# Kernel optimization log

Hardware: AMD Instinct MI355X
Metric: run time of the kernel (lower is better)

Reference implementation:

```python
import jax, jax.numpy as jnp
import numpy as np

V, D, B, L, Dh, BS = 50257, 1024, 8, 2, 128, 256

def setup_inputs() -> dict:
    key = jax.random.key(0)
    ks = jax.random.split(key, 16)
    std = lambda fan: 1.0 / np.sqrt(fan)
    return {
        'input_id': jax.random.randint(ks[0], (BS,), 0, V),
        'reset_mask': jax.random.randint(ks[1], (BS,), 0, 2).astype(bool),
        'surprise': jnp.zeros((BS, 1), jnp.float32),
        'wm_state': jax.random.normal(ks[2], (BS, D), jnp.float32) * 0.1,
        'h_state': jax.random.normal(ks[3], (L, BS, B, Dh), jnp.float32) * 0.1,
        'emb': jax.random.normal(ks[4], (V, D), jnp.float32) * std(D),
        'W_in': jax.random.normal(ks[5], (D, D), jnp.float32) * std(D),
        'W_alpha': jax.random.normal(ks[6], (D, D), jnp.float32) * std(D),
        'W_wm_out': jax.random.normal(ks[7], (D, D), jnp.float32) * std(D),
        'W_x': jax.random.normal(ks[8], (L, B, Dh, Dh), jnp.float32) * std(Dh),
        'W_h': jax.random.normal(ks[9], (L, B, Dh, Dh), jnp.float32) * std(Dh),
        'W_wml': jax.random.normal(ks[10], (L, B, Dh, D), jnp.float32) * std(D),
        'W_g': jax.random.normal(ks[11], (L, B, Dh, Dh), jnp.float32) * std(Dh),
        'w_s': jnp.zeros((L, B, Dh), jnp.float32),   # surprise gate weights (init 0, as in torch init)
        'b_g': jnp.zeros((L, B, Dh), jnp.float32),   # gate bias
    }


def reference(input_id, reset_mask, surprise, wm_state, h_state, emb, W_in,
              W_alpha, W_wm_out, W_x, W_h, W_wml, W_g, w_s, b_g):
    # carry = (~reset_mask) as float, zeroes all recurrent state at doc boundary
    carry = (~reset_mask).astype(jnp.float32)[:, None]            # [BS,1]
    x = emb[input_id]                                             # [BS,D] token embedding
    # GLA-style working memory: input-conditioned decay of carried state
    alpha = jax.nn.sigmoid(x @ W_alpha.T)                         # [BS,D]
    wm_new = carry * alpha * wm_state + x                         # [BS,D]
    y_wm = jnp.tanh(wm_new @ W_wm_out.T)                          # [BS,D]
    # input projection and split into B block slices of width D_h
    x_proj = x @ W_in.T                                           # [BS,D]
    cur = x_proj.reshape(BS, B, Dh)                               # [BS,B,Dh]
    carry_b = carry[:, :, None]                                   # [BS,1,1]
    # L sequential layers per block; all B blocks updated in parallel via einsum
    for l in range(L):
        a = (jnp.einsum('sbd,bed->sbe', cur, W_x[l])
             + jnp.einsum('sbd,bed->sbe', h_state[l], W_h[l])
             + jnp.einsum('sD,beD->sbe', y_wm, W_wml[l]))         # [BS,B,Dh]
        g = jax.nn.sigmoid(jnp.einsum('sbd,bed->sbe', a, W_g[l])
                           + surprise[:, :, None] * w_s[l] + b_g[l])
        h_new = carry_b * ((1.0 - g) * h_state[l] + g * jnp.tanh(a))
        cur = h_new
    h_final = cur.reshape(BS, D)                                  # concat of per-block outputs
    logits = h_final @ emb.T                                      # tied lm_head
    return logits, x, y_wm
```

## Files before the change

### kernel.cpp

```cpp
#include <hip/hip_runtime.h>
#include <math.h>

#define BSZ 256
#define DIM 1024
#define VOC 50257
#define NL 2
#define NB 8
#define DH 128

typedef __bf16 bf16x8 __attribute__((ext_vector_type(8)));
typedef float  f32x4  __attribute__((ext_vector_type(4)));
typedef unsigned short u16;
typedef u16 u16x8 __attribute__((ext_vector_type(8)));

__device__ __forceinline__ u16 f2bf(float f) {
  unsigned int u = __float_as_uint(f);
  u += 0x7fffu + ((u >> 16) & 1u);
  return (u16)(u >> 16);
}
__device__ __forceinline__ float sigm(float x) { return 1.0f / (1.0f + __expf(-x)); }

template<int M16, int N16, int K, bool CLAMPN>
__device__ __forceinline__ void wave_gemm(
    const u16* __restrict__ A, int lda,
    const float* __restrict__ B, int ldb, int nClamp,
    f32x4 (&acc)[M16][N16])
{
  const int lane = threadIdx.x & 63;
  const int quad = lane >> 4;
  const int l16  = lane & 15;

  const u16* aR[M16];
  const float* bR[N16];
#pragma unroll
  for (int mi = 0; mi < M16; ++mi)
    aR[mi] = A + (long)(mi * 16 + l16) * lda + quad * 8;
#pragma unroll
  for (int ni = 0; ni < N16; ++ni) {
    int n = ni * 16 + l16;
    if (CLAMPN) n = n > nClamp ? nClamp : n;
    bR[ni] = B + (long)n * ldb + quad * 8;
  }

  bf16x8 aF[4][M16];
  bf16x8 bF[4][N16];

#define WG_LOAD(kk, buf)                                                  \
  {                                                                       \
    _Pragma("unroll")                                                     \
    for (int ni = 0; ni < N16; ++ni) {                                    \
      float4 v0 = *(const float4*)(bR[ni] + (kk));                        \
      float4 v1 = *(const float4*)(bR[ni] + (kk) + 4);                    \
      u16x8 h;                                                            \
      h[0] = f2bf(v0.x); h[1] = f2bf(v0.y);                               \
      h[2] = f2bf(v0.z); h[3] = f2bf(v0.w);                               \
      h[4] = f2bf(v1.x); h[5] = f2bf(v1.y);                               \
      h[6] = f2bf(v1.z); h[7] = f2bf(v1.w);                               \
      bF[buf][ni] = __builtin_bit_cast(bf16x8, h);                        \
    }                                                                     \
    _Pragma("unroll")                                                     \
    for (int mi = 0; mi < M16; ++mi)                                      \
      aF[buf][mi] = *(const bf16x8*)(aR[mi] + (kk));                      \
  }

#define WG_MM(buf)                                                        \
  {                                                                       \
    _Pragma("unroll")                                                     \
    for (int mi = 0; mi < M16; ++mi)                                      \
      _Pragma("unroll")                                                   \
      for (int ni = 0; ni < N16; ++ni)                                    \
        acc[mi][ni] = __builtin_amdgcn_mfma_f32_16x16x32_bf16(            \
            aF[buf][mi], bF[buf][ni], acc[mi][ni], 0, 0, 0);              \
  }

  WG_LOAD(0, 0);
  WG_LOAD(32, 1);
  WG_LOAD(64, 2);
#pragma unroll 1
  for (int kk = 0; kk < K - 128; kk += 128) {
    WG_LOAD(kk + 96, 3);  WG_MM(0);
    WG_LOAD(kk + 128, 0); WG_MM(1);
    WG_LOAD(kk + 160, 1); WG_MM(2);
    WG_LOAD(kk + 192, 2); WG_MM(3);
  }
  WG_LOAD(K - 32, 3);
  WG_MM(0); WG_MM(1); WG_MM(2); WG_MM(3);
#undef WG_LOAD
#undef WG_MM
}

#define ACC_DECL(N16V)                                \
  f32x4 acc[4][N16V];                                 \
  { f32x4 z = {0.f, 0.f, 0.f, 0.f};                   \
    _Pragma("unroll")                                 \
    for (int i = 0; i < 4; ++i)                       \
      _Pragma("unroll")                               \
      for (int j = 0; j < N16V; ++j) acc[i][j] = z; }

__global__ __launch_bounds__(256) void k_prep(
    const int* __restrict__ ids, const void* __restrict__ mask,
    const float* __restrict__ emb, const float* __restrict__ hstate,
    const float* __restrict__ W_alpha, const float* __restrict__ W_in,
    const float* __restrict__ W_wm_out, const float* __restrict__ W_x,
    const float* __restrict__ W_h, const float* __restrict__ W_wml,
    const float* __restrict__ W_g,
    float* __restrict__ xout, u16* __restrict__ x_bf,
    u16* __restrict__ h_bf, float* __restrict__ carry, float* __restrict__ sink)
{
  __shared__ int sInt;
  const int tid = threadIdx.x, s = blockIdx.x;
  if (tid == 0) sInt = 1;
  __syncthreads();
  if (tid < 64) {
    int v = ((const int*)mask)[tid];
    if (v != 0 && v != 1) atomicAnd(&sInt, 0);
  }
  __syncthreads();
  if (tid == 0) {
    int m = sInt ? ((const int*)mask)[s] : (int)((const unsigned char*)mask)[s];
    carry[s] = m ? 0.0f : 1.0f;
  }
  long id = ids[s];
  int k = tid * 4;
  float4 v = *(const float4*)(emb + id * DIM + k);
  *(float4*)(xout + (long)s * DIM + k) = v;
  ushort4 h; h.x = f2bf(v.x); h.y = f2bf(v.y); h.z = f2bf(v.z); h.w = f2bf(v.w);
  *(ushort4*)(x_bf + (long)s * DIM + k) = h;
#pragma unroll
  for (int l = 0; l < NL; ++l) {
    long off = (long)l * BSZ * DIM + (long)s * DIM + k;
    float4 w = *(const float4*)(hstate + off);
    ushort4 o; o.x = f2bf(w.x); o.y = f2bf(w.y); o.z = f2bf(w.z); o.w = f2bf(w.w);
    *(ushort4*)(h_bf + off) = o;
  }
  long gtid = (long)blockIdx.x * 256 + tid;
  long gstride = (long)gridDim.x * 256;
  float acc = 0.f;
  {
    const long nDD = (long)DIM * DIM / 4;
    for (long i = gtid; i < nDD; i += gstride) {
      float4 a = ((const float4*)W_alpha)[i];
      float4 b = ((const float4*)W_in)[i];
      float4 c = ((const float4*)W_wm_out)[i];
      acc += a.x + a.w + b.x + b.w + c.x + c.w;
    }
    const long nS = (long)NL * NB * DH * DH / 4;
    for (long i = gtid; i < nS; i += gstride) {
      float4 a = ((const float4*)W_x)[i];
      float4 b = ((const float4*)W_h)[i];
      float4 c = ((const float4*)W_g)[i];
      acc += a.x + a.w + b.x + b.w + c.x + c.w;
    }
    const long nW = (long)NL * NB * DH * DIM / 4;
    for (long i = gtid; i < nW; i += gstride) {
      float4 a = ((const float4*)W_wml)[i];
      acc += a.x + a.w;
    }
  }
  if (acc == -1.17521e35f) *sink = acc;
}

__global__ __launch_bounds__(64) void k_gemm1(
    const u16* __restrict__ x_bf,
    const float* __restrict__ W_alpha, const float* __restrict__ W_in,
    const float* __restrict__ carry, const float* __restrict__ wm_state,
    const float* __restrict__ xout,
    u16* __restrict__ wm_bf, u16* __restrict__ cur_bf)
{
  const int tid = threadIdx.x, quad = tid >> 4, l16 = tid & 15;
  const int m = blockIdx.x & 3;
  const int nt = blockIdx.x >> 2;
  const bool isAlpha = nt < 64;
  const int n0 = (isAlpha ? nt : nt - 64) * 16;
  ACC_DECL(1)
  wave_gemm<4, 1, DIM, false>(x_bf + (long)m * 64 * DIM, DIM,
                              (isAlpha ? W_alpha : W_in) + (long)n0 * DIM, DIM, 0, acc);
#pragma unroll
  for (int mi = 0; mi < 4; ++mi) {
    int n = n0 + l16;
#pragma unroll
    for (int r = 0; r < 4; ++r) {
      int s = m * 64 + mi * 16 + quad * 4 + r;
      float c = acc[mi][0][r];
      long idx = (long)s * DIM + n;
      if (isAlpha) wm_bf[idx] = f2bf(carry[s] * sigm(c) * wm_state[idx] + xout[idx]);
      else         cur_bf[idx] = f2bf(c);
    }
  }
}

__global__ __launch_bounds__(64) void k_gemm2(
    const u16* __restrict__ wm_bf, const float* __restrict__ W_wm_out,
    float* __restrict__ yout, u16* __restrict__ ywm_bf)
{
  const int tid = threadIdx.x, quad = tid >> 4, l16 = tid & 15;
  const int m = blockIdx.x & 3;
  const int n0 = (blockIdx.x >> 2) * 16;
  ACC_DECL(1)
  wave_gemm<4, 1, DIM, false>(wm_bf + (long)m * 64 * DIM, DIM,
                              W_wm_out + (long)n0 * DIM, DIM, 0, acc);
#pragma unroll
  for (int mi = 0; mi < 4; ++mi) {
    int n = n0 + l16;
#pragma unroll
    for (int r = 0; r < 4; ++r) {
      int s = m * 64 + mi * 16 + quad * 4 + r;
      float y = tanhf(acc[mi][0][r]);
      long idx = (long)s * DIM + n;
      yout[idx] = y;
      ywm_bf[idx] = f2bf(y);
    }
  }
}

__global__ __launch_bounds__(64) void k_gemm_a(
    int l, const u16* __restrict__ cur_bf, const u16* __restrict__ h_bf,
    const u16* __restrict__ ywm_bf,
    const float* __restrict__ W_x, const float* __restrict__ W_h,
    const float* __restrict__ W_wml,
    float* __restrict__ a_f32, u16* __restrict__ a_bf)
{
  const int tid = threadIdx.x, quad = tid >> 4, l16 = tid & 15;
  const int m = blockIdx.x & 3;
  const int nt = blockIdx.x >> 2;
  const int b = nt >> 3;
  const int e0 = (nt & 7) * 16;
  ACC_DECL(1)
  const long moff = (long)m * 64 * DIM;
  wave_gemm<4, 1, DH, false>(cur_bf + moff + b * DH, DIM,
                             W_x + ((long)(l * NB + b) * DH + e0) * DH, DH, 0, acc);
  wave_gemm<4, 1, DH, false>(h_bf + (long)l * BSZ * DIM + moff + b * DH, DIM,
                             W_h + ((long)(l * NB + b) * DH + e0) * DH, DH, 0, acc);
  wave_gemm<4, 1, DIM, false>(ywm_bf + moff, DIM,
                              W_wml + ((long)(l * NB + b) * DH + e0) * DIM, DIM, 0, acc);
#pragma unroll
  for (int mi = 0; mi < 4; ++mi) {
    int e = e0 + l16;
#pragma unroll
    for (int r = 0; r < 4; ++r) {
      int s = m * 64 + mi * 16 + quad * 4 + r;
      float c = acc[mi][0][r];
      long idx = (long)s * DIM + b * DH + e;
      a_f32[idx] = c;
      a_bf[idx] = f2bf(c);
    }
  }
}

__global__ __launch_bounds__(64) void k_gemm_g(
    int l, const u16* __restrict__ a_bf, const float* __restrict__ W_g,
    const float* __restrict__ w_s, const float* __restrict__ b_g,
    const float* __restrict__ surprise, const float* __restrict__ carry,
    const float* __restrict__ hstate, const float* __restrict__ a_f32,
    u16* __restrict__ hout_bf)
{
  const int tid = threadIdx.x, quad = tid >> 4, l16 = tid & 15;
  const int m = blockIdx.x & 3;
  const int nt = blockIdx.x >> 2;
  const int b = nt >> 3;
  const int e0 = (nt & 7) * 16;
  ACC_DECL(1)
  wave_gemm<4, 1, DH, false>(a_bf + (long)m * 64 * DIM + b * DH, DIM,
                             W_g + ((long)(l * NB + b) * DH + e0) * DH, DH, 0, acc);
#pragma unroll
  for (int mi = 0; mi < 4; ++mi) {
    int e = e0 + l16;
#pragma unroll
    for (int r = 0; r < 4; ++r) {
      int s = m * 64 + mi * 16 + quad * 4 + r;
      float c = acc[mi][0][r];
      long idx = (long)s * DIM + b * DH + e;
      float gp = c + surprise[s] * w_s[(l * NB + b) * DH + e] + b_g[(l * NB + b) * DH + e];
      float g = sigm(gp);
      float ho = hstate[(long)l * BSZ * DIM + idx];
      float hn = carry[s] * ((1.0f - g) * ho + g * tanhf(a_f32[idx]));
      hout_bf[idx] = f2bf(hn);
    }
  }
}

__global__ __launch_bounds__(256) void k_logits_lds(
    const u16* __restrict__ hfin_bf, const float* __restrict__ emb,
    float* __restrict__ out)
{
  __shared__ u16 Bs[2][64 * 64];
  const int tid  = threadIdx.x;
  const int wave = tid >> 6;
  const int lane = tid & 63;
  const int quad = lane >> 4;
  const int l16  = lane & 15;
  const int n0   = blockIdx.x * 64;

  const int srow = tid >> 2;
  const int scol = (tid & 3) * 16;
  long gn = n0 + srow;
  if (gn >= VOC) gn = VOC - 1;
  const float* src = emb + gn * DIM + scol;
  const int sw  = (srow & 7) << 4;
  const int sb0 = srow * 128 + ((scol * 2) ^ sw);
  const int sb1 = srow * 128 + (((scol * 2) + 16) ^ sw);

  const u16* aP[4];
#pragma unroll
  for (int mi = 0; mi < 4; ++mi)
    aP[mi] = hfin_bf + (long)(wave * 64 + mi * 16 + l16) * DIM + quad * 8;

  f32x4 acc[4][4];
  { f32x4 z = {0.f, 0.f, 0.f, 0.f};
#pragma unroll
    for (int mi = 0; mi < 4; ++mi)
#pragma unroll
      for (int ni = 0; ni < 4; ++ni) acc[mi][ni] = z; }

  float4 pA, pB, pC, pD;
#define LD4(t)                                                            \
  { pA = *(const float4*)(src + (t) * 64);                                \
    pB = *(const float4*)(src + (t) * 64 + 4);                            \
    pC = *(const float4*)(src + (t) * 64 + 8);                            \
    pD = *(const float4*)(src + (t) * 64 + 12); }
#define CVT_WR(bufi)                                                      \
  { u16x8 h0, h1;                                                         \
    h0[0] = f2bf(pA.x); h0[1] = f2bf(pA.y);                               \
    h0[2] = f2bf(pA.z); h0[3] = f2bf(pA.w);                               \
    h0[4] = f2bf(pB.x); h0[5] = f2bf(pB.y);                               \
    h0[6] = f2bf(pB.z); h0[7] = f2bf(pB.w);                               \
    h1[0] = f2bf(pC.x); h1[1] = f2bf(pC.y);                               \
    h1[2] = f2bf(pC.z); h1[3] = f2bf(pC.w);                               \
    h1[4] = f2bf(pD.x); h1[5] = f2bf(pD.y);                               \
    h1[6] = f2bf(pD.z); h1[7] = f2bf(pD.w);                               \
    *(u16x8*)((char*)&Bs[bufi][0] + sb0) = h0;                            \
    *(u16x8*)((char*)&Bs[bufi][0] + sb1) = h1; }

  LD4(0)
  CVT_WR(0)
  LD4(1)
  __syncthreads();

  const int NT = DIM / 64;
#pragma unroll 1
  for (int t = 0; t < NT; ++t) {
    const char* bb = (const char*)&Bs[t & 1][0];
    const int k0 = t * 64;

    bf16x8 aF0[4], aF1[4], bF0[4], bF1[4];
#pragma unroll
    for (int mi = 0; mi < 4; ++mi) aF0[mi] = *(const bf16x8*)(aP[mi] + k0);
#pragma unroll
    for (int mi = 0; mi < 4; ++mi) aF1[mi] = *(const bf16x8*)(aP[mi] + k0 + 32);
#pragma unroll
    for (int ni = 0; ni < 4; ++ni) {
      const int row = ni * 16 + l16;
      const int ib0 = (quad * 16) ^ ((row & 7) << 4);
      bF0[ni] = *(const bf16x8*)(bb + row * 128 + ib0);
      bF1[ni] = *(const bf16x8*)(bb + row * 128 + (ib0 ^ 64));
    }
#pragma unroll
    for (int mi = 0; mi < 4; ++mi)
#pragma unroll
      for (int ni = 0; ni < 4; ++ni)
        acc[mi][ni] = __builtin_amdgcn_mfma_f32_16x16x32_bf16(
            aF0[mi], bF0[ni], acc[mi][ni], 0, 0, 0);
#pragma unroll
    for (int mi = 0; mi < 4; ++mi)
#pragma unroll
      for (int ni = 0; ni < 4; ++ni)
        acc[mi][ni] = __builtin_amdgcn_mfma_f32_16x16x32_bf16(
            aF1[mi], bF1[ni], acc[mi][ni], 0, 0, 0);

    if (t + 1 < NT) {
      CVT_WR((t + 1) & 1)
      if (t + 2 < NT) LD4(t + 2)
    }
    __syncthreads();
  }
#undef LD4
#undef CVT_WR

#pragma unroll
  for (int mi = 0; mi < 4; ++mi)
#pragma unroll
    for (int ni = 0; ni < 4; ++ni) {
      int n = n0 + ni * 16 + l16;
      if (n < VOC) {
#pragma unroll
        for (int r = 0; r < 4; ++r) {
          int s = wave * 64 + mi * 16 + quad * 4 + r;
          out[(long)s * VOC + n] = acc[mi][ni][r];
        }
      }
    }
}

extern "C" void kernel_launch(void* const* d_in, const int* in_sizes, int n_in,
                              void* d_out, int out_size, void* d_ws, size_t ws_size,
                              hipStream_t stream) {
  const int*   input_id = (const int*)d_in[0];
  const void*  reset    = d_in[1];
  const float* surprise = (const float*)d_in[2];
  const float* wm_state = (const float*)d_in[3];
  const float* h_state  = (const float*)d_in[4];
  const float* emb      = (const float*)d_in[5];
  const float* W_in     = (const float*)d_in[6];
  const float* W_alpha  = (const float*)d_in[7];
  const float* W_wm_out = (const float*)d_in[8];
  const float* W_x      = (const float*)d_in[9];
  const float* W_h      = (const float*)d_in[10];
  const float* W_wml    = (const float*)d_in[11];
  const float* W_g      = (const float*)d_in[12];
  const float* w_s      = (const float*)d_in[13];
  const float* b_g      = (const float*)d_in[14];

  float* out  = (float*)d_out;
  float* xout = out + (size_t)BSZ * VOC;
  float* yout = xout + (size_t)BSZ * DIM;

  const long SD = (long)BSZ * DIM;
  u16* scr    = (u16*)d_out;
  u16* x_bf   = scr;
  u16* wm_bf  = scr + SD;
  u16* cur_bf = scr + 2 * SD;
  u16* ywm_bf = scr + 3 * SD;
  u16* h_bf   = scr + 4 * SD;
  u16* a_bf   = scr + 6 * SD;
  float* a_f32 = (float*)(scr + 8 * SD);

  float* carry  = (float*)d_ws;
  u16* hfin_bf  = (u16*)((char*)d_ws + 1024);
  float* sink   = (float*)((char*)d_ws + 600 * 1024);

  k_prep<<<BSZ, 256, 0, stream>>>(input_id, reset, emb, h_state,
                                  W_alpha, W_in, W_wm_out, W_x, W_h, W_wml, W_g,
                                  xout, x_bf, h_bf, carry, sink);
  k_gemm1<<<512, 64, 0, stream>>>(x_bf, W_alpha, W_in, carry, wm_state, xout, wm_bf, cur_bf);
  k_gemm2<<<256, 64, 0, stream>>>(wm_bf, W_wm_out, yout, ywm_bf);
  k_gemm_a<<<256, 64, 0, stream>>>(0, cur_bf, h_bf, ywm_bf, W_x, W_h, W_wml, a_f32, a_bf);
  k_gemm_g<<<256, 64, 0, stream>>>(0, a_bf, W_g, w_s, b_g, surprise, carry, h_state, a_f32, cur_bf);
  k_gemm_a<<<256, 64, 0, stream>>>(1, cur_bf, h_bf, ywm_bf, W_x, W_h, W_wml, a_f32, a_bf);
  k_gemm_g<<<256, 64, 0, stream>>>(1, a_bf, W_g, w_s, b_g, surprise, carry, h_state, a_f32, hfin_bf);
  k_logits_lds<<<(VOC + 63) / 64, 256, 0, stream>>>(hfin_bf, emb, out);
}
```

Measured before the change: 461.1 us.

## Fuse both recurrent layers into one LDS-resident kernel; deepen logits prefetch

Replaces the four per-layer gate/activation kernels with one k_layers kernel. Each 512-thread block owns 16 rows of one block slice and keeps cur, a and h in LDS across both layers, so the global a_f32/a_bf round trips and three launches go away. The logits kernel's loop is unrolled by two with two register prefetch sets, so emb loads are issued two tiles ahead. The trade-off is fewer blocks (128) and smaller M tiles that reload weights per row-group, plus higher register pressure in the logits kernel.

```diff
diff --git a/kernel.cpp b/kernel.cpp
--- a/kernel.cpp
+++ b/kernel.cpp
@@ -89,6 +89,27 @@
 #undef WG_MM
 }
 
+__device__ __forceinline__ void wave_gemm_ldsA(
+    const u16* S, const float* __restrict__ B, int ldb, f32x4& acc,
+    int l16, int quad)
+{
+  const float* bR = B + (long)l16 * ldb + quad * 8;
+#pragma unroll
+  for (int c = 0; c < 4; ++c) {
+    bf16x8 af = *(const bf16x8*)((const char*)S + l16 * 256 +
+                                 ((c * 64 + quad * 16) ^ ((l16 & 7) << 4)));
+    float4 v0 = *(const float4*)(bR + c * 32);
+    float4 v1 = *(const float4*)(bR + c * 32 + 4);
+    u16x8 h;
+    h[0] = f2bf(v0.x); h[1] = f2bf(v0.y);
+    h[2] = f2bf(v0.z); h[3] = f2bf(v0.w);
+    h[4] = f2bf(v1.x); h[5] = f2bf(v1.y);
+    h[6] = f2bf(v1.z); h[7] = f2bf(v1.w);
+    acc = __builtin_amdgcn_mfma_f32_16x16x32_bf16(
+        af, __builtin_bit_cast(bf16x8, h), acc, 0, 0, 0);
+  }
+}
+
 #define ACC_DECL(N16V)                                \
   f32x4 acc[4][N16V];                                 \
   { f32x4 z = {0.f, 0.f, 0.f, 0.f};                   \
@@ -213,69 +234,75 @@
   }
 }
 
-__global__ __launch_bounds__(64) void k_gemm_a(
-    int l, const u16* __restrict__ cur_bf, const u16* __restrict__ h_bf,
+__global__ __launch_bounds__(512) void k_layers(
+    const u16* __restrict__ cur_bf, const u16* __restrict__ h_bf,
     const u16* __restrict__ ywm_bf,
     const float* __restrict__ W_x, const float* __restrict__ W_h,
-    const float* __restrict__ W_wml,
-    float* __restrict__ a_f32, u16* __restrict__ a_bf)
-{
-  const int tid = threadIdx.x, quad = tid >> 4, l16 = tid & 15;
-  const int m = blockIdx.x & 3;
-  const int nt = blockIdx.x >> 2;
-  const int b = nt >> 3;
-  const int e0 = (nt & 7) * 16;
-  ACC_DECL(1)
-  const long moff = (long)m * 64 * DIM;
-  wave_gemm<4, 1, DH, false>(cur_bf + moff + b * DH, DIM,
-                             W_x + ((long)(l * NB + b) * DH + e0) * DH, DH, 0, acc);
-  wave_gemm<4, 1, DH, false>(h_bf + (long)l * BSZ * DIM + moff + b * DH, DIM,
-                             W_h + ((long)(l * NB + b) * DH + e0) * DH, DH, 0, acc);
-  wave_gemm<4, 1, DIM, false>(ywm_bf + moff, DIM,
-                              W_wml + ((long)(l * NB + b) * DH + e0) * DIM, DIM, 0, acc);
-#pragma unroll
-  for (int mi = 0; mi < 4; ++mi) {
-    int e = e0 + l16;
-#pragma unroll
-    for (int r = 0; r < 4; ++r) {
-      int s = m * 64 + mi * 16 + quad * 4 + r;
-      float c = acc[mi][0][r];
-      long idx = (long)s * DIM + b * DH + e;
-      a_f32[idx] = c;
-      a_bf[idx] = f2bf(c);
-    }
-  }
-}
-
-__global__ __launch_bounds__(64) void k_gemm_g(
-    int l, const u16* __restrict__ a_bf, const float* __restrict__ W_g,
+    const float* __restrict__ W_wml, const float* __restrict__ W_g,
     const float* __restrict__ w_s, const float* __restrict__ b_g,
     const float* __restrict__ surprise, const float* __restrict__ carry,
-    const float* __restrict__ hstate, const float* __restrict__ a_f32,
-    u16* __restrict__ hout_bf)
-{
-  const int tid = threadIdx.x, quad = tid >> 4, l16 = tid & 15;
-  const int m = blockIdx.x & 3;
-  const int nt = blockIdx.x >> 2;
-  const int b = nt >> 3;
-  const int e0 = (nt & 7) * 16;
-  ACC_DECL(1)
-  wave_gemm<4, 1, DH, false>(a_bf + (long)m * 64 * DIM + b * DH, DIM,
-                             W_g + ((long)(l * NB + b) * DH + e0) * DH, DH, 0, acc);
-#pragma unroll
-  for (int mi = 0; mi < 4; ++mi) {
-    int e = e0 + l16;
+    const float* __restrict__ hstate,
+    u16* __restrict__ hfin_bf)
+{
+  __shared__ u16 S[16 * 128];
+  const int tid  = threadIdx.x;
+  const int wv   = tid >> 6;
+  const int lane = tid & 63;
+  const int quad = lane >> 4, l16 = lane & 15;
+  const int m  = blockIdx.x & 15;
+  const int b  = blockIdx.x >> 4;
+  const int e0 = wv * 16;
+  const int row0 = m * 16;
+
+  {
+    const int r  = tid >> 5;
+    const int c8 = (tid & 31) * 8;
+    uint2 v = *(const uint2*)((const char*)(cur_bf + (long)(row0 + r) * DIM + b * DH) + c8);
+    *(uint2*)((char*)S + r * 256 + (c8 ^ ((r & 7) << 4))) = v;
+  }
+  __syncthreads();
+
+#pragma unroll 1
+  for (int l = 0; l < NL; ++l) {
+    const long wb = (long)(l * NB + b) * DH;
+    f32x4 aacc[1][1];
+    { f32x4 z = {0.f, 0.f, 0.f, 0.f}; aacc[0][0] = z; }
+    wave_gemm_ldsA(S, W_x + (wb + e0) * DH, DH, aacc[0][0], l16, quad);
+    wave_gemm<1, 1, DH, false>(h_bf + (long)l * BSZ * DIM + (long)row0 * DIM + b * DH, DIM,
+                               W_h + (wb + e0) * DH, DH, 0, aacc);
+    wave_gemm<1, 1, DIM, false>(ywm_bf + (long)row0 * DIM, DIM,
+                                W_wml + (wb + e0) * DIM, DIM, 0, aacc);
+    __syncthreads();
 #pragma unroll
     for (int r = 0; r < 4; ++r) {
-      int s = m * 64 + mi * 16 + quad * 4 + r;
-      float c = acc[mi][0][r];
-      long idx = (long)s * DIM + b * DH + e;
-      float gp = c + surprise[s] * w_s[(l * NB + b) * DH + e] + b_g[(l * NB + b) * DH + e];
-      float g = sigm(gp);
-      float ho = hstate[(long)l * BSZ * DIM + idx];
-      float hn = carry[s] * ((1.0f - g) * ho + g * tanhf(a_f32[idx]));
-      hout_bf[idx] = f2bf(hn);
-    }
+      int row = quad * 4 + r;
+      *(u16*)((char*)S + row * 256 + (((e0 + l16) * 2) ^ ((row & 7) << 4))) =
+          f2bf(aacc[0][0][r]);
+    }
+    __syncthreads();
+    f32x4 gacc = {0.f, 0.f, 0.f, 0.f};
+    wave_gemm_ldsA(S, W_g + (wb + e0) * DH, DH, gacc, l16, quad);
+    const int col = e0 + l16;
+    const float ws_v = w_s[wb + col];
+    const float bg_v = b_g[wb + col];
+    float hn[4];
+#pragma unroll
+    for (int r = 0; r < 4; ++r) {
+      int s = row0 + quad * 4 + r;
+      float g = sigm(gacc[r] + surprise[s] * ws_v + bg_v);
+      float ho = hstate[(long)l * BSZ * DIM + (long)s * DIM + b * DH + col];
+      hn[r] = carry[s] * ((1.0f - g) * ho + g * tanhf(aacc[0][0][r]));
+    }
+    __syncthreads();
+#pragma unroll
+    for (int r = 0; r < 4; ++r) {
+      int row = quad * 4 + r;
+      u16 hv = f2bf(hn[r]);
+      *(u16*)((char*)S + row * 256 + ((col * 2) ^ ((row & 7) << 4))) = hv;
+      if (l == NL - 1)
+        hfin_bf[(long)(row0 + row) * DIM + b * DH + col] = hv;
+    }
+    __syncthreads();
   }
 }
 
@@ -312,69 +339,82 @@
 #pragma unroll
       for (int ni = 0; ni < 4; ++ni) acc[mi][ni] = z; }
 
-  float4 pA, pB, pC, pD;
-#define LD4(t)                                                            \
-  { pA = *(const float4*)(src + (t) * 64);                                \
-    pB = *(const float4*)(src + (t) * 64 + 4);                            \
-    pC = *(const float4*)(src + (t) * 64 + 8);                            \
-    pD = *(const float4*)(src + (t) * 64 + 12); }
-#define CVT_WR(bufi)                                                      \
+  float4 P0, P1, P2, P3, Q0, Q1, Q2, Q3;
+#define LDP(t)                                                            \
+  { P0 = *(const float4*)(src + (t) * 64);                                \
+    P1 = *(const float4*)(src + (t) * 64 + 4);                            \
+    P2 = *(const float4*)(src + (t) * 64 + 8);                            \
+    P3 = *(const float4*)(src + (t) * 64 + 12); }
+#define LDQ(t)                                                            \
+  { Q0 = *(const float4*)(src + (t) * 64);                                \
+    Q1 = *(const float4*)(src + (t) * 64 + 4);                            \
+    Q2 = *(const float4*)(src + (t) * 64 + 8);                            \
+    Q3 = *(const float4*)(src + (t) * 64 + 12); }
+#define CVT_WR(bufi, a, bq, c, d)                                         \
   { u16x8 h0, h1;                                                         \
-    h0[0] = f2bf(pA.x); h0[1] = f2bf(pA.y);                               \
-    h0[2] = f2bf(pA.z); h0[3] = f2bf(pA.w);                               \
-    h0[4] = f2bf(pB.x); h0[5] = f2bf(pB.y);                               \
-    h0[6] = f2bf(pB.z); h0[7] = f2bf(pB.w);                               \
-    h1[0] = f2bf(pC.x); h1[1] = f2bf(pC.y);                               \
-    h1[2] = f2bf(pC.z); h1[3] = f2bf(pC.w);                               \
-    h1[4] = f2bf(pD.x); h1[5] = f2bf(pD.y);                               \
-    h1[6] = f2bf(pD.z); h1[7] = f2bf(pD.w);                               \
+    h0[0] = f2bf(a.x); h0[1] = f2bf(a.y);                                 \
+    h0[2] = f2bf(a.z); h0[3] = f2bf(a.w);                                 \
+    h0[4] = f2bf(bq.x); h0[5] = f2bf(bq.y);                               \
+    h0[6] = f2bf(bq.z); h0[7] = f2bf(bq.w);                               \
+    h1[0] = f2bf(c.x); h1[1] = f2bf(c.y);                                 \
+    h1[2] = f2bf(c.z); h1[3] = f2bf(c.w);                                 \
+    h1[4] = f2bf(d.x); h1[5] = f2bf(d.y);                                 \
+    h1[6] = f2bf(d.z); h1[7] = f2bf(d.w);                                 \
     *(u16x8*)((char*)&Bs[bufi][0] + sb0) = h0;                            \
     *(u16x8*)((char*)&Bs[bufi][0] + sb1) = h1; }
-
-  LD4(0)
-  CVT_WR(0)
-  LD4(1)
+#define COMPUTE(t, bufi)                                                  \
+  { const char* bb = (const char*)&Bs[bufi][0];                           \
+    const int k0 = (t) * 64;                                              \
+    bf16x8 aF0[4], aF1[4], bF0[4], bF1[4];                                \
+    _Pragma("unroll")                                                     \
+    for (int mi = 0; mi < 4; ++mi) aF0[mi] = *(const bf16x8*)(aP[mi] + k0);\
+    _Pragma("unroll")                                                     \
+    for (int mi = 0; mi < 4; ++mi) aF1[mi] = *(const bf16x8*)(aP[mi] + k0 + 32);\
+    _Pragma("unroll")                                                     \
+    for (int ni = 0; ni < 4; ++ni) {                                      \
+      const int row = ni * 16 + l16;                                      \
+      const int ib0 = (quad * 16) ^ ((row & 7) << 4);                     \
+      bF0[ni] = *(const bf16x8*)(bb + row * 128 + ib0);                   \
+      bF1[ni] = *(const bf16x8*)(bb + row * 128 + (ib0 ^ 64));            \
+    }                                                                     \
+    _Pragma("unroll")                                                     \
+    for (int mi = 0; mi < 4; ++mi)                                        \
+      _Pragma("unroll")                                                   \
+      for (int ni = 0; ni < 4; ++ni)                                      \
+        acc[mi][ni] = __builtin_amdgcn_mfma_f32_16x16x32_bf16(            \
+            aF0[mi], bF0[ni], acc[mi][ni], 0, 0, 0);                      \
+    _Pragma("unroll")                                                     \
+    for (int mi = 0; mi < 4; ++mi)                                        \
+      _Pragma("unroll")                                                   \
+      for (int ni = 0; ni < 4; ++ni)                                      \
+        acc[mi][ni] = __builtin_amdgcn_mfma_f32_16x16x32_bf16(            \
+            aF1[mi], bF1[ni], acc[mi][ni], 0, 0, 0);                      \
+  }
+
+  LDP(0)
+  CVT_WR(0, P0, P1, P2, P3)
+  LDP(1)
+  LDQ(2)
   __syncthreads();
 
   const int NT = DIM / 64;
 #pragma unroll 1
-  for (int t = 0; t < NT; ++t) {
-    const char* bb = (const char*)&Bs[t & 1][0];
-    const int k0 = t * 64;
-
-    bf16x8 aF0[4], aF1[4], bF0[4], bF1[4];
-#pragma unroll
-    for (int mi = 0; mi < 4; ++mi) aF0[mi] = *(const bf16x8*)(aP[mi] + k0);
-#pragma unroll
-    for (int mi = 0; mi < 4; ++mi) aF1[mi] = *(const bf16x8*)(aP[mi] + k0 + 32);
-#pragma unroll
-    for (int ni = 0; ni < 4; ++ni) {
-      const int row = ni * 16 + l16;
-      const int ib0 = (quad * 16) ^ ((row & 7) << 4);
-      bF0[ni] = *(const bf16x8*)(bb + row * 128 + ib0);
-      bF1[ni] = *(const bf16x8*)(bb + row * 128 + (ib0 ^ 64));
-    }
-#pragma unroll
-    for (int mi = 0; mi < 4; ++mi)
-#pragma unroll
-      for (int ni = 0; ni < 4; ++ni)
-        acc[mi][ni] = __builtin_amdgcn_mfma_f32_16x16x32_bf16(
-            aF0[mi], bF0[ni], acc[mi][ni], 0, 0, 0);
-#pragma unroll
-    for (int mi = 0; mi < 4; ++mi)
-#pragma unroll
-      for (int ni = 0; ni < 4; ++ni)
-        acc[mi][ni] = __builtin_amdgcn_mfma_f32_16x16x32_bf16(
-            aF1[mi], bF1[ni], acc[mi][ni], 0, 0, 0);
-
-    if (t + 1 < NT) {
-      CVT_WR((t + 1) & 1)
-      if (t + 2 < NT) LD4(t + 2)
-    }
-    __syncthreads();
-  }
-#undef LD4
+  for (int t = 0; t < NT; t += 2) {
+    COMPUTE(t, 0)
+    CVT_WR(1, P0, P1, P2, P3)
+    if (t + 3 < NT) LDP(t + 3)
+    __syncthreads();
+    COMPUTE(t + 1, 1)
+    if (t + 2 < NT) {
+      CVT_WR(0, Q0, Q1, Q2, Q3)
+      if (t + 4 < NT) LDQ(t + 4)
+    }
+    __syncthreads();
+  }
+#undef LDP
+#undef LDQ
 #undef CVT_WR
+#undef COMPUTE
 
 #pragma unroll
   for (int mi = 0; mi < 4; ++mi)
@@ -421,8 +461,6 @@
   u16* cur_bf = scr + 2 * SD;
   u16* ywm_bf = scr + 3 * SD;
   u16* h_bf   = scr + 4 * SD;
-  u16* a_bf   = scr + 6 * SD;
-  float* a_f32 = (float*)(scr + 8 * SD);
 
   float* carry  = (float*)d_ws;
   u16* hfin_bf  = (u16*)((char*)d_ws + 1024);
@@ -433,9 +471,7 @@
                                   xout, x_bf, h_bf, carry, sink);
   k_gemm1<<<512, 64, 0, stream>>>(x_bf, W_alpha, W_in, carry, wm_state, xout, wm_bf, cur_bf);
   k_gemm2<<<256, 64, 0, stream>>>(wm_bf, W_wm_out, yout, ywm_bf);
-  k_gemm_a<<<256, 64, 0, stream>>>(0, cur_bf, h_bf, ywm_bf, W_x, W_h, W_wml, a_f32, a_bf);
-  k_gemm_g<<<256, 64, 0, stream>>>(0, a_bf, W_g, w_s, b_g, surprise, carry, h_state, a_f32, cur_bf);
-  k_gemm_a<<<256, 64, 0, stream>>>(1, cur_bf, h_bf, ywm_bf, W_x, W_h, W_wml, a_f32, a_bf);
-  k_gemm_g<<<256, 64, 0, stream>>>(1, a_bf, W_g, w_s, b_g, surprise, carry, h_state, a_f32, hfin_bf);
+  k_layers<<<128, 512, 0, stream>>>(cur_bf, h_bf, ywm_bf, W_x, W_h, W_wml, W_g,
+                                    w_s, b_g, surprise, carry, h_state, hfin_bf);
   k_logits_lds<<<(VOC + 63) / 64, 256, 0, stream>>>(hfin_bf, emb, out);
 }
```

New measurement: 482.7 us. +4.7%, slower.

## Stage fp32 embedding tiles into LDS with direct global-to-LDS loads in logits GEMM

Applied to the files above, without the earlier changes.

The logits kernel now copies fp32 embedding tiles straight into LDS through global_load_lds (16 bytes per lane) using an XOR swizzle. The bf16 conversion moves to the point where B fragments are read from LDS. This removes the register round trip and the conversion-then-store step from the prefetch path, and lets the next tile's load be issued before the current tile's MFMAs. In exchange LDS use doubles (fp32 tiles), each wave does more LDS reads and conversions per MFMA, and the double-buffer sync relies on the barrier covering the asynchronous LDS writes.

```diff
diff --git a/kernel.cpp b/kernel.cpp
--- a/kernel.cpp
+++ b/kernel.cpp
@@ -11,6 +11,7 @@
 typedef __bf16 bf16x8 __attribute__((ext_vector_type(8)));
 typedef float  f32x4  __attribute__((ext_vector_type(4)));
 typedef unsigned short u16;
+typedef unsigned int u32;
 typedef u16 u16x8 __attribute__((ext_vector_type(8)));
 
 __device__ __forceinline__ u16 f2bf(float f) {
@@ -19,6 +20,19 @@
   return (u16)(u >> 16);
 }
 __device__ __forceinline__ float sigm(float x) { return 1.0f / (1.0f + __expf(-x)); }
+
+__device__ __forceinline__ bf16x8 cvt8(float4 a, float4 b) {
+  bf16x8 r;
+  r[0] = (__bf16)a.x; r[1] = (__bf16)a.y; r[2] = (__bf16)a.z; r[3] = (__bf16)a.w;
+  r[4] = (__bf16)b.x; r[5] = (__bf16)b.y; r[6] = (__bf16)b.z; r[7] = (__bf16)b.w;
+  return r;
+}
+
+__device__ __forceinline__ void gld16(const float* g, float* l) {
+  __builtin_amdgcn_global_load_lds(
+      (const __attribute__((address_space(1))) u32*)(g),
+      (__attribute__((address_space(3))) u32*)(l), 16, 0, 0);
+}
 
 template<int M16, int N16, int K, bool CLAMPN>
 __device__ __forceinline__ void wave_gemm(
@@ -279,11 +293,11 @@
   }
 }
 
-__global__ __launch_bounds__(256) void k_logits_lds(
+__global__ __launch_bounds__(256) void k_logits_gl(
     const u16* __restrict__ hfin_bf, const float* __restrict__ emb,
     float* __restrict__ out)
 {
-  __shared__ u16 Bs[2][64 * 64];
+  __shared__ float Bs[2][64 * 64];
   const int tid  = threadIdx.x;
   const int wave = tid >> 6;
   const int lane = tid & 63;
@@ -291,14 +305,15 @@
   const int l16  = lane & 15;
   const int n0   = blockIdx.x * 64;
 
-  const int srow = tid >> 2;
-  const int scol = (tid & 3) * 16;
-  long gn = n0 + srow;
-  if (gn >= VOC) gn = VOC - 1;
-  const float* src = emb + gn * DIM + scol;
-  const int sw  = (srow & 7) << 4;
-  const int sb0 = srow * 128 + ((scol * 2) ^ sw);
-  const int sb1 = srow * 128 + (((scol * 2) + 16) ^ sw);
+  const float* srcP[4];
+#pragma unroll
+  for (int j = 0; j < 4; ++j) {
+    int r = wave * 16 + j * 4 + (lane >> 4);
+    int c = (lane & 15) ^ (r & 15);
+    long gn = n0 + r; if (gn > VOC - 1) gn = VOC - 1;
+    srcP[j] = emb + gn * DIM + c * 4;
+  }
+  float* const dst0 = &Bs[0][wave * 16 * 64];
 
   const u16* aP[4];
 #pragma unroll
@@ -312,47 +327,36 @@
 #pragma unroll
       for (int ni = 0; ni < 4; ++ni) acc[mi][ni] = z; }
 
-  float4 pA, pB, pC, pD;
-#define LD4(t)                                                            \
-  { pA = *(const float4*)(src + (t) * 64);                                \
-    pB = *(const float4*)(src + (t) * 64 + 4);                            \
-    pC = *(const float4*)(src + (t) * 64 + 8);                            \
-    pD = *(const float4*)(src + (t) * 64 + 12); }
-#define CVT_WR(bufi)                                                      \
-  { u16x8 h0, h1;                                                         \
-    h0[0] = f2bf(pA.x); h0[1] = f2bf(pA.y);                               \
-    h0[2] = f2bf(pA.z); h0[3] = f2bf(pA.w);                               \
-    h0[4] = f2bf(pB.x); h0[5] = f2bf(pB.y);                               \
-    h0[6] = f2bf(pB.z); h0[7] = f2bf(pB.w);                               \
-    h1[0] = f2bf(pC.x); h1[1] = f2bf(pC.y);                               \
-    h1[2] = f2bf(pC.z); h1[3] = f2bf(pC.w);                               \
-    h1[4] = f2bf(pD.x); h1[5] = f2bf(pD.y);                               \
-    h1[6] = f2bf(pD.z); h1[7] = f2bf(pD.w);                               \
-    *(u16x8*)((char*)&Bs[bufi][0] + sb0) = h0;                            \
-    *(u16x8*)((char*)&Bs[bufi][0] + sb1) = h1; }
-
-  LD4(0)
-  CVT_WR(0)
-  LD4(1)
+#define STAGE(bufi, t)                                                    \
+  { _Pragma("unroll")                                                     \
+    for (int j = 0; j < 4; ++j)                                           \
+      gld16(srcP[j] + (t) * 64, dst0 + (bufi) * 4096 + j * 256); }
+
+  STAGE(0, 0)
   __syncthreads();
 
   const int NT = DIM / 64;
 #pragma unroll 1
   for (int t = 0; t < NT; ++t) {
+    const int k0 = t * 64;
+    bf16x8 aF0[4], aF1[4];
+#pragma unroll
+    for (int mi = 0; mi < 4; ++mi) aF0[mi] = *(const bf16x8*)(aP[mi] + k0);
+#pragma unroll
+    for (int mi = 0; mi < 4; ++mi) aF1[mi] = *(const bf16x8*)(aP[mi] + k0 + 32);
+    if (t + 1 < NT) { STAGE((t + 1) & 1, t + 1) }
+
     const char* bb = (const char*)&Bs[t & 1][0];
-    const int k0 = t * 64;
-
-    bf16x8 aF0[4], aF1[4], bF0[4], bF1[4];
-#pragma unroll
-    for (int mi = 0; mi < 4; ++mi) aF0[mi] = *(const bf16x8*)(aP[mi] + k0);
-#pragma unroll
-    for (int mi = 0; mi < 4; ++mi) aF1[mi] = *(const bf16x8*)(aP[mi] + k0 + 32);
+    bf16x8 bF0[4], bF1[4];
 #pragma unroll
     for (int ni = 0; ni < 4; ++ni) {
-      const int row = ni * 16 + l16;
-      const int ib0 = (quad * 16) ^ ((row & 7) << 4);
-      bF0[ni] = *(const bf16x8*)(bb + row * 128 + ib0);
-      bF1[ni] = *(const bf16x8*)(bb + row * 128 + (ib0 ^ 64));
+      const char* rb = bb + (ni * 16 + l16) * 256;
+      float4 u0 = *(const float4*)(rb + (((quad * 2)     ^ l16) << 4));
+      float4 u1 = *(const float4*)(rb + (((quad * 2 + 1) ^ l16) << 4));
+      float4 w0 = *(const float4*)(rb + (((quad * 2 + 8) ^ l16) << 4));
+      float4 w1 = *(const float4*)(rb + (((quad * 2 + 9) ^ l16) << 4));
+      bF0[ni] = cvt8(u0, u1);
+      bF1[ni] = cvt8(w0, w1);
     }
 #pragma unroll
     for (int mi = 0; mi < 4; ++mi)
@@ -367,14 +371,9 @@
         acc[mi][ni] = __builtin_amdgcn_mfma_f32_16x16x32_bf16(
             aF1[mi], bF1[ni], acc[mi][ni], 0, 0, 0);
 
-    if (t + 1 < NT) {
-      CVT_WR((t + 1) & 1)
-      if (t + 2 < NT) LD4(t + 2)
-    }
     __syncthreads();
   }
-#undef LD4
-#undef CVT_WR
+#undef STAGE
 
 #pragma unroll
   for (int mi = 0; mi < 4; ++mi)
@@ -437,5 +436,5 @@
   k_gemm_g<<<256, 64, 0, stream>>>(0, a_bf, W_g, w_s, b_g, surprise, carry, h_state, a_f32, cur_bf);
   k_gemm_a<<<256, 64, 0, stream>>>(1, cur_bf, h_bf, ywm_bf, W_x, W_h, W_wml, a_f32, a_bf);
   k_gemm_g<<<256, 64, 0, stream>>>(1, a_bf, W_g, w_s, b_g, surprise, carry, h_state, a_f32, hfin_bf);
-  k_logits_lds<<<(VOC + 63) / 64, 256, 0, stream>>>(hfin_bf, emb, out);
-}
+  k_logits_gl<<<(VOC + 63) / 64, 256, 0, stream>>>(hfin_bf, emb, out);
+}
```

Result: no change. 453.7 us (-1.6%).
